# Kernel optimization log

Hardware: AMD Instinct MI355X
Metric: run time of the kernel (lower is better)

The kernel has to match this reference:

```python
import jax, jax.numpy as jnp
import numpy as np

HEADS = 8
DIM_HEAD = 64
DIM = 512
INNER = HEADS * DIM_HEAD  # 512
SCALE = DIM_HEAD ** -0.5


def setup_inputs() -> dict:
    key = jax.random.key(0)
    k1, k2, k3, k4 = jax.random.split(key, 4)
    B, N = 2, 4096
    x = jax.random.normal(k1, (B, N, DIM), dtype=jnp.float32)
    # nn.Linear(dim, inner*3, bias=False): weight [3*inner, dim]; y = x @ W.T
    w_qkv = jax.random.normal(k2, (3 * INNER, DIM), dtype=jnp.float32) * (DIM ** -0.5)
    w_out = jax.random.normal(k3, (DIM, INNER), dtype=jnp.float32) * (INNER ** -0.5)
    b_out = jax.random.normal(k4, (DIM,), dtype=jnp.float32) * 0.01
    return {"x": x, "w_qkv": w_qkv, "w_out": w_out, "b_out": b_out, "H": 64, "W": 64}


def reference(x, w_qkv, w_out, b_out, H, W):
    B, N, _ = x.shape
    qkv = jnp.einsum('bnd,ed->bne', x, w_qkv)  # [B, N, 3*inner]
    q, k, v = jnp.split(qkv, 3, axis=-1)
    def to_heads(t):
        return t.reshape(B, N, HEADS, DIM_HEAD).transpose(0, 2, 1, 3)  # b h n d
    q, k, v = to_heads(q), to_heads(k), to_heads(v)
    dots = jnp.einsum('bhid,bhjd->bhij', q, k) * SCALE
    attn = jax.nn.softmax(dots, axis=-1)  # dropout p=0.0 -> identity
    out = jnp.einsum('bhij,bhjd->bhid', attn, v)
    out = out.transpose(0, 2, 1, 3).reshape(B, N, INNER)
    return jnp.einsum('bne,de->bnd', out, w_out) + b_out
```

## Files before the change

kernel.cpp:

```cpp
#include <hip/hip_runtime.h>
#include <hip/hip_bf16.h>

typedef __hip_bfloat16 bf16;
typedef __attribute__((ext_vector_type(8))) short short8;
typedef __attribute__((ext_vector_type(4))) short shortx4;
typedef __attribute__((ext_vector_type(4))) float floatx4;
typedef __attribute__((ext_vector_type(4))) int intx4;

#define MFMA16(a, b, c) __builtin_amdgcn_mfma_f32_16x16x32_bf16((a), (b), (c), 0, 0, 0)
#define EXP2(x) __builtin_amdgcn_exp2f(x)

__device__ __forceinline__ short f2s(float v) {
    return __builtin_bit_cast(short, __float2bfloat16(v));
}

__device__ __forceinline__ int packhi(float lo, float hi) {
    return (int)__builtin_amdgcn_perm(__builtin_bit_cast(unsigned, hi),
                                      __builtin_bit_cast(unsigned, lo),
                                      0x07060302u);
}

__device__ __forceinline__ short8 cvt8v(float4 f0, float4 f1) {
    short8 r;
    r[0] = f2s(f0.x); r[1] = f2s(f0.y); r[2] = f2s(f0.z); r[3] = f2s(f0.w);
    r[4] = f2s(f1.x); r[5] = f2s(f1.y); r[6] = f2s(f1.z); r[7] = f2s(f1.w);
    return r;
}

__global__ __launch_bounds__(256) void qkv_gemm(
    const float* __restrict__ x, const float* __restrict__ wq,
    bf16* __restrict__ q, bf16* __restrict__ k, bf16* __restrict__ vt)
{
    __shared__ short pool[20480];
    short (*As)[128][40] = (short(*)[128][40])pool;
    short (*Bs)[128][40] = (short(*)[128][40])(pool + 10240);
    short (*Vt)[136] = (short(*)[136])pool;
    const int t = threadIdx.x;
    const int bm = blockIdx.x * 128;
    const int be = blockIdx.y * 128;
    const int w = t >> 6, lane = t & 63, lq = lane >> 4, lm = lane & 15;
    const int wr = w >> 1, wc = w & 1;
    const int srow = t >> 1, scol = (t & 1) * 16;
    const float C = 0.18033688011112042f;

    const float* xp = &x[(size_t)(bm + srow) * 512 + scol];
    const float* wp = &wq[(size_t)(be + srow) * 512 + scol];

    float4 xr[4], wr4[4];
    auto issue = [&](int k0) {
        const float4* a = (const float4*)(xp + k0);
        const float4* b = (const float4*)(wp + k0);
        xr[0] = a[0]; xr[1] = a[1]; xr[2] = a[2]; xr[3] = a[3];
        wr4[0] = b[0]; wr4[1] = b[1]; wr4[2] = b[2]; wr4[3] = b[3];
    };
    auto commit = [&](int buf) {
        *(short8*)&As[buf][srow][scol]     = cvt8v(xr[0], xr[1]);
        *(short8*)&As[buf][srow][scol + 8] = cvt8v(xr[2], xr[3]);
        *(short8*)&Bs[buf][srow][scol]     = cvt8v(wr4[0], wr4[1]);
        *(short8*)&Bs[buf][srow][scol + 8] = cvt8v(wr4[2], wr4[3]);
    };

    floatx4 acc[4][4];
#pragma unroll
    for (int i = 0; i < 4; ++i)
#pragma unroll
        for (int j = 0; j < 4; ++j) acc[i][j] = {0.f, 0.f, 0.f, 0.f};

    issue(0);
    commit(0);
    __syncthreads();
    int cur = 0;
    for (int k0 = 0; k0 < 512; k0 += 32) {
        const bool more = (k0 + 32) < 512;
        if (more) issue(k0 + 32);
        short8 af[4], bf[4];
#pragma unroll
        for (int mt = 0; mt < 4; ++mt) af[mt] = *(const short8*)&As[cur][wr * 64 + mt * 16 + lm][lq * 8];
#pragma unroll
        for (int nt = 0; nt < 4; ++nt) bf[nt] = *(const short8*)&Bs[cur][wc * 64 + nt * 16 + lm][lq * 8];
#pragma unroll
        for (int mt = 0; mt < 4; ++mt)
#pragma unroll
            for (int nt = 0; nt < 4; ++nt)
                acc[mt][nt] = MFMA16(af[mt], bf[nt], acc[mt][nt]);
        if (more) {
            commit(cur ^ 1);
            __syncthreads();
        }
        cur ^= 1;
    }

    const int which = be >> 9;
    if (which < 2) {
#pragma unroll
        for (int nt = 0; nt < 4; ++nt) {
            const int gcol = be + wc * 64 + nt * 16 + lm;
            const int e2 = gcol & 511;
            const int h = e2 >> 6, d = e2 & 63;
#pragma unroll
            for (int mt = 0; mt < 4; ++mt) {
#pragma unroll
                for (int r = 0; r < 4; ++r) {
                    int grow = bm + wr * 64 + mt * 16 + lq * 4 + r;
                    int b = grow >> 12, n = grow & 4095;
                    int bh = b * 8 + h;
                    float v = acc[mt][nt][r];
                    if (which == 0)
                        q[((size_t)bh * 4096 + n) * 64 + d] = __float2bfloat16(v * C);
                    else
                        k[((size_t)bh * 4096 + n) * 64 + d] = __float2bfloat16(v);
                }
            }
        }
    } else {
        __syncthreads();
#pragma unroll
        for (int nt = 0; nt < 4; ++nt) {
            const int e_loc = wc * 64 + nt * 16 + lm;
#pragma unroll
            for (int mt = 0; mt < 4; ++mt) {
                const int col = wr * 64 + 4 * (mt & 1) + 8 * lq + 32 * (mt >> 1);
                shortx4 v4;
#pragma unroll
                for (int r = 0; r < 4; ++r) v4[r] = f2s(acc[mt][nt][r]);
                *(shortx4*)&Vt[e_loc][col] = v4;
            }
        }
        __syncthreads();
        const int b = bm >> 12, n0 = bm & 4095;
        const int h0 = (be - 1024) >> 6;
        const int row = t >> 1, cb = (t & 1) * 64;
        const int h = h0 + (row >> 6), d = row & 63;
        const size_t gb = ((size_t)(b * 8 + h) * 64 + d) * 4096 + n0 + cb;
#pragma unroll
        for (int c = 0; c < 8; ++c)
            *(intx4*)&vt[gb + c * 8] = *(const intx4*)&Vt[row][cb + c * 8];
    }
}

__global__ __launch_bounds__(256, 2) void flash_attn(
    const bf16* __restrict__ q, const bf16* __restrict__ k,
    const bf16* __restrict__ vt, bf16* __restrict__ out)
{
    __shared__ short Qs[128][72];
    __shared__ short Ks[2][64][72];
    __shared__ short Vs[2][64][72];
    const int t = threadIdx.x;
    const int i0 = blockIdx.x * 128;
    const int bh = blockIdx.y;
    const int w = t >> 6, lane = t & 63, lq = lane >> 4, lm = lane & 15;
    const floatx4 zero4 = {0.f, 0.f, 0.f, 0.f};

    const size_t nbase = (size_t)bh * 4096 * 64;
    const size_t vbase = (size_t)bh * 64 * 4096;
    const int r0 = t >> 3, c0 = (t & 7) * 8;

#pragma unroll
    for (int it = 0; it < 4; ++it) {
        int off = it * 2048 + t * 8;
        int row = off >> 6, col = off & 63;
        *(intx4*)&Qs[row][col] = *(const intx4*)&q[nbase + (size_t)(i0 + row) * 64 + col];
    }

    intx4 kreg[2], vreg[2];
    auto issue = [&](int j0n) {
        kreg[0] = *(const intx4*)&k[nbase + (size_t)(j0n + r0) * 64 + c0];
        kreg[1] = *(const intx4*)&k[nbase + (size_t)(j0n + 32 + r0) * 64 + c0];
        vreg[0] = *(const intx4*)&vt[vbase + (size_t)r0 * 4096 + j0n + c0];
        vreg[1] = *(const intx4*)&vt[vbase + (size_t)(32 + r0) * 4096 + j0n + c0];
    };
    auto commit = [&](int buf) {
        *(intx4*)&Ks[buf][r0][c0]      = kreg[0];
        *(intx4*)&Ks[buf][32 + r0][c0] = kreg[1];
        *(intx4*)&Vs[buf][r0][c0]      = vreg[0];
        *(intx4*)&Vs[buf][32 + r0][c0] = vreg[1];
    };

    issue(0);
    commit(0);
    __syncthreads();
    short8 aq0[2], aq1[2];
#pragma unroll
    for (int g = 0; g < 2; ++g) {
        aq0[g] = *(const short8*)&Qs[g * 64 + w * 16 + lm][lq * 8];
        aq1[g] = *(const short8*)&Qs[g * 64 + w * 16 + lm][32 + lq * 8];
    }

    float l_lane[2] = {0.f, 0.f};
    floatx4 o_acc[2][4];
#pragma unroll
    for (int g = 0; g < 2; ++g)
#pragma unroll
        for (int dt = 0; dt < 4; ++dt) o_acc[g][dt] = zero4;

    int cur = 0;
    for (int j0 = 0; j0 < 4096; j0 += 64) {
        const bool more = (j0 + 64) < 4096;
        if (more) issue(j0 + 64);

        floatx4 s[2][4];
#pragma unroll
        for (int jt = 0; jt < 4; ++jt) {
            short8 bk0 = *(const short8*)&Ks[cur][jt * 16 + lm][lq * 8];
            short8 bk1 = *(const short8*)&Ks[cur][jt * 16 + lm][32 + lq * 8];
#pragma unroll
            for (int g = 0; g < 2; ++g) {
                s[g][jt] = MFMA16(bk0, aq0[g], zero4);
                s[g][jt] = MFMA16(bk1, aq1[g], s[g][jt]);
            }
        }

        short8 bp0[2], bp1[2];
#pragma unroll
        for (int g = 0; g < 2; ++g) {
            intx4 pkA, pkB;
#pragma unroll
            for (int jt = 0; jt < 4; ++jt) {
                float e0 = EXP2(s[g][jt][0]);
                float e1 = EXP2(s[g][jt][1]);
                float e2 = EXP2(s[g][jt][2]);
                float e3 = EXP2(s[g][jt][3]);
                l_lane[g] += (e0 + e1) + (e2 + e3);
                if (jt < 2) {
                    pkA[jt * 2]     = packhi(e0, e1);
                    pkA[jt * 2 + 1] = packhi(e2, e3);
                } else {
                    pkB[(jt - 2) * 2]     = packhi(e0, e1);
                    pkB[(jt - 2) * 2 + 1] = packhi(e2, e3);
                }
            }
            bp0[g] = __builtin_bit_cast(short8, pkA);
            bp1[g] = __builtin_bit_cast(short8, pkB);
        }

#pragma unroll
        for (int dt = 0; dt < 4; ++dt) {
            short8 av0 = *(const short8*)&Vs[cur][dt * 16 + lm][lq * 8];
            short8 av1 = *(const short8*)&Vs[cur][dt * 16 + lm][32 + lq * 8];
#pragma unroll
            for (int g = 0; g < 2; ++g) {
                o_acc[g][dt] = MFMA16(av0, bp0[g], o_acc[g][dt]);
                o_acc[g][dt] = MFMA16(av1, bp1[g], o_acc[g][dt]);
            }
        }

        if (more) {
            commit(cur ^ 1);
            __syncthreads();
        }
        cur ^= 1;
    }

    const int b = bh >> 3, h = bh & 7;
    short* Os = (short*)Qs;
    const int obase = w * 1024;
    const int il = lane >> 2, c = (lane & 3) * 16;
#pragma unroll
    for (int g = 0; g < 2; ++g) {
        float l = l_lane[g];
        l += __shfl_xor(l, 16);
        l += __shfl_xor(l, 32);
        const float inv_l = 1.0f / l;
        __syncthreads();
#pragma unroll
        for (int dt = 0; dt < 4; ++dt)
#pragma unroll
            for (int r = 0; r < 4; ++r)
                Os[obase + lm * 64 + dt * 16 + lq * 4 + r] = f2s(o_acc[g][dt][r] * inv_l);
        __syncthreads();
        const int i = i0 + g * 64 + w * 16 + il;
        intx4 v0 = *(const intx4*)&Os[obase + il * 64 + c];
        intx4 v1 = *(const intx4*)&Os[obase + il * 64 + c + 8];
        *(intx4*)&out[((size_t)b * 4096 + i) * 512 + h * 64 + c] = v0;
        *(intx4*)&out[((size_t)b * 4096 + i) * 512 + h * 64 + c + 8] = v1;
    }
}

__global__ __launch_bounds__(256) void out_gemm(
    const bf16* __restrict__ a, const float* __restrict__ wo,
    const float* __restrict__ bias, float* __restrict__ y)
{
    __shared__ short As[2][128][40];
    __shared__ short Bs[2][64][40];
    const int t = threadIdx.x;
    const int bm = blockIdx.x * 128;
    const int be = blockIdx.y * 64;
    const int w = t >> 6, lane = t & 63, lq = lane >> 4, lm = lane & 15;
    const int wr = w >> 1, wc = w & 1;
    const int srow = t >> 1, scol = (t & 1) * 16;
    const int brow = t >> 2, bcol = (t & 3) * 8;

    const bf16* ap = &a[(size_t)(bm + srow) * 512 + scol];
    const float* wp = &wo[(size_t)(be + brow) * 512 + bcol];

    intx4 ar[2];
    float4 br[2];
    auto issue = [&](int k0) {
        ar[0] = *(const intx4*)(ap + k0);
        ar[1] = *(const intx4*)(ap + k0 + 8);
        br[0] = ((const float4*)(wp + k0))[0];
        br[1] = ((const float4*)(wp + k0))[1];
    };
    auto commit = [&](int buf) {
        *(intx4*)&As[buf][srow][scol]     = ar[0];
        *(intx4*)&As[buf][srow][scol + 8] = ar[1];
        *(short8*)&Bs[buf][brow][bcol]    = cvt8v(br[0], br[1]);
    };

    floatx4 acc[4][2];
#pragma unroll
    for (int i = 0; i < 4; ++i)
#pragma unroll
        for (int j = 0; j < 2; ++j) acc[i][j] = {0.f, 0.f, 0.f, 0.f};

    issue(0);
    commit(0);
    __syncthreads();
    int cur = 0;
    for (int k0 = 0; k0 < 512; k0 += 32) {
        const bool more = (k0 + 32) < 512;
        if (more) issue(k0 + 32);
        short8 af[4], bf[2];
#pragma unroll
        for (int mt = 0; mt < 4; ++mt) af[mt] = *(const short8*)&As[cur][wr * 64 + mt * 16 + lm][lq * 8];
#pragma unroll
        for (int nt = 0; nt < 2; ++nt) bf[nt] = *(const short8*)&Bs[cur][wc * 32 + nt * 16 + lm][lq * 8];
#pragma unroll
        for (int mt = 0; mt < 4; ++mt)
#pragma unroll
            for (int nt = 0; nt < 2; ++nt)
                acc[mt][nt] = MFMA16(af[mt], bf[nt], acc[mt][nt]);
        if (more) {
            commit(cur ^ 1);
            __syncthreads();
        }
        cur ^= 1;
    }

#pragma unroll
    for (int nt = 0; nt < 2; ++nt) {
        const int gcol = be + wc * 32 + nt * 16 + lm;
        const float bv = bias[gcol];
#pragma unroll
        for (int mt = 0; mt < 4; ++mt) {
#pragma unroll
            for (int r = 0; r < 4; ++r) {
                int grow = bm + wr * 64 + mt * 16 + lq * 4 + r;
                y[(size_t)grow * 512 + gcol] = acc[mt][nt][r] + bv;
            }
        }
    }
}

extern "C" void kernel_launch(void* const* d_in, const int* in_sizes, int n_in,
                              void* d_out, int out_size, void* d_ws, size_t ws_size,
                              hipStream_t stream) {
    const float* x     = (const float*)d_in[0];
    const float* w_qkv = (const float*)d_in[1];
    const float* w_out = (const float*)d_in[2];
    const float* b_out = (const float*)d_in[3];

    const size_t HEAD_ELEMS = (size_t)16 * 4096 * 64;
    bf16* qw  = (bf16*)d_ws;
    bf16* kw  = qw + HEAD_ELEMS;
    bf16* vtw = kw + HEAD_ELEMS;
    bf16* aw  = vtw + HEAD_ELEMS;
    float* y  = (float*)d_out;

    qkv_gemm<<<dim3(64, 12), 256, 0, stream>>>(x, w_qkv, qw, kw, vtw);
    flash_attn<<<dim3(32, 16), 256, 0, stream>>>(qw, kw, vtw, aw);
    out_gemm<<<dim3(64, 8), 256, 0, stream>>>(aw, w_out, b_out, y);
}
```

Baseline: 204.6 us.

## Stage Q/K epilogue through LDS and deepen register prefetch to two tiles

The QKV GEMM epilogue for Q and K now writes the accumulator tile into shared memory and then stores whole 128-byte rows with 16-byte vector stores, replacing scattered 2-byte global writes. The attention and output-GEMM main loops keep two register stages of prefetched K/V (or A/W) data, so global loads are issued two iterations ahead instead of one. The aim is to raise store coalescing and hide more global-load latency, at the cost of extra registers (possible occupancy loss) and one extra barrier in the epilogue.

```diff
diff --git a/kernel.cpp b/kernel.cpp
--- a/kernel.cpp
+++ b/kernel.cpp
@@ -34,6 +34,7 @@
     __shared__ short pool[20480];
     short (*As)[128][40] = (short(*)[128][40])pool;
     short (*Bs)[128][40] = (short(*)[128][40])(pool + 10240);
+    short (*Qt)[144] = (short(*)[144])pool;
     short (*Vt)[136] = (short(*)[136])pool;
     const int t = threadIdx.x;
     const int bm = blockIdx.x * 128;
@@ -91,29 +92,29 @@
     }
 
     const int which = be >> 9;
+    __syncthreads();
     if (which < 2) {
+        const float scale = (which == 0) ? C : 1.0f;
 #pragma unroll
         for (int nt = 0; nt < 4; ++nt) {
-            const int gcol = be + wc * 64 + nt * 16 + lm;
-            const int e2 = gcol & 511;
-            const int h = e2 >> 6, d = e2 & 63;
-#pragma unroll
-            for (int mt = 0; mt < 4; ++mt) {
-#pragma unroll
-                for (int r = 0; r < 4; ++r) {
-                    int grow = bm + wr * 64 + mt * 16 + lq * 4 + r;
-                    int b = grow >> 12, n = grow & 4095;
-                    int bh = b * 8 + h;
-                    float v = acc[mt][nt][r];
-                    if (which == 0)
-                        q[((size_t)bh * 4096 + n) * 64 + d] = __float2bfloat16(v * C);
-                    else
-                        k[((size_t)bh * 4096 + n) * 64 + d] = __float2bfloat16(v);
-                }
-            }
-        }
+            const int e_loc = wc * 64 + nt * 16 + lm;
+#pragma unroll
+            for (int mt = 0; mt < 4; ++mt)
+#pragma unroll
+                for (int r = 0; r < 4; ++r)
+                    Qt[wr * 64 + mt * 16 + lq * 4 + r][e_loc] = f2s(acc[mt][nt][r] * scale);
+        }
+        __syncthreads();
+        bf16* dst = (which == 0) ? q : k;
+        const int tr = t >> 1, th = t & 1;
+        const int grow = bm + tr;
+        const int b = grow >> 12, n = grow & 4095;
+        const int h = ((be + th * 64) & 511) >> 6;
+        bf16* p = dst + ((size_t)(b * 8 + h) * 4096 + n) * 64;
+#pragma unroll
+        for (int c = 0; c < 8; ++c)
+            *(intx4*)&p[c * 8] = *(const intx4*)&Qt[tr][th * 64 + c * 8];
     } else {
-        __syncthreads();
 #pragma unroll
         for (int nt = 0; nt < 4; ++nt) {
             const int e_loc = wc * 64 + nt * 16 + lm;
@@ -162,22 +163,23 @@
         *(intx4*)&Qs[row][col] = *(const intx4*)&q[nbase + (size_t)(i0 + row) * 64 + col];
     }
 
-    intx4 kreg[2], vreg[2];
-    auto issue = [&](int j0n) {
-        kreg[0] = *(const intx4*)&k[nbase + (size_t)(j0n + r0) * 64 + c0];
-        kreg[1] = *(const intx4*)&k[nbase + (size_t)(j0n + 32 + r0) * 64 + c0];
-        vreg[0] = *(const intx4*)&vt[vbase + (size_t)r0 * 4096 + j0n + c0];
-        vreg[1] = *(const intx4*)&vt[vbase + (size_t)(32 + r0) * 4096 + j0n + c0];
-    };
-    auto commit = [&](int buf) {
-        *(intx4*)&Ks[buf][r0][c0]      = kreg[0];
-        *(intx4*)&Ks[buf][32 + r0][c0] = kreg[1];
-        *(intx4*)&Vs[buf][r0][c0]      = vreg[0];
-        *(intx4*)&Vs[buf][32 + r0][c0] = vreg[1];
-    };
-
-    issue(0);
-    commit(0);
+    intx4 kreg[2][2], vreg[2][2];
+    auto issue = [&](int j0n, int s) {
+        kreg[s][0] = *(const intx4*)&k[nbase + (size_t)(j0n + r0) * 64 + c0];
+        kreg[s][1] = *(const intx4*)&k[nbase + (size_t)(j0n + 32 + r0) * 64 + c0];
+        vreg[s][0] = *(const intx4*)&vt[vbase + (size_t)r0 * 4096 + j0n + c0];
+        vreg[s][1] = *(const intx4*)&vt[vbase + (size_t)(32 + r0) * 4096 + j0n + c0];
+    };
+    auto commit = [&](int s, int buf) {
+        *(intx4*)&Ks[buf][r0][c0]      = kreg[s][0];
+        *(intx4*)&Ks[buf][32 + r0][c0] = kreg[s][1];
+        *(intx4*)&Vs[buf][r0][c0]      = vreg[s][0];
+        *(intx4*)&Vs[buf][32 + r0][c0] = vreg[s][1];
+    };
+
+    issue(0, 0);
+    commit(0, 0);
+    issue(64, 1);
     __syncthreads();
     short8 aq0[2], aq1[2];
 #pragma unroll
@@ -193,10 +195,10 @@
 #pragma unroll
         for (int dt = 0; dt < 4; ++dt) o_acc[g][dt] = zero4;
 
-    int cur = 0;
-    for (int j0 = 0; j0 < 4096; j0 += 64) {
-        const bool more = (j0 + 64) < 4096;
-        if (more) issue(j0 + 64);
+    for (int i = 0; i < 64; ++i) {
+        const int j0 = i * 64;
+        const int cur = i & 1;
+        if (j0 + 128 < 4096) issue(j0 + 128, cur);
 
         floatx4 s[2][4];
 #pragma unroll
@@ -244,11 +246,10 @@
             }
         }
 
-        if (more) {
-            commit(cur ^ 1);
+        if (j0 + 64 < 4096) {
+            commit(cur ^ 1, cur ^ 1);
             __syncthreads();
         }
-        cur ^= 1;
     }
 
     const int b = bh >> 3, h = bh & 7;
@@ -293,18 +294,18 @@
     const bf16* ap = &a[(size_t)(bm + srow) * 512 + scol];
     const float* wp = &wo[(size_t)(be + brow) * 512 + bcol];
 
-    intx4 ar[2];
-    float4 br[2];
-    auto issue = [&](int k0) {
-        ar[0] = *(const intx4*)(ap + k0);
-        ar[1] = *(const intx4*)(ap + k0 + 8);
-        br[0] = ((const float4*)(wp + k0))[0];
-        br[1] = ((const float4*)(wp + k0))[1];
-    };
-    auto commit = [&](int buf) {
-        *(intx4*)&As[buf][srow][scol]     = ar[0];
-        *(intx4*)&As[buf][srow][scol + 8] = ar[1];
-        *(short8*)&Bs[buf][brow][bcol]    = cvt8v(br[0], br[1]);
+    intx4 ar[2][2];
+    float4 br[2][2];
+    auto issue = [&](int k0, int s) {
+        ar[s][0] = *(const intx4*)(ap + k0);
+        ar[s][1] = *(const intx4*)(ap + k0 + 8);
+        br[s][0] = ((const float4*)(wp + k0))[0];
+        br[s][1] = ((const float4*)(wp + k0))[1];
+    };
+    auto commit = [&](int s, int buf) {
+        *(intx4*)&As[buf][srow][scol]     = ar[s][0];
+        *(intx4*)&As[buf][srow][scol + 8] = ar[s][1];
+        *(short8*)&Bs[buf][brow][bcol]    = cvt8v(br[s][0], br[s][1]);
     };
 
     floatx4 acc[4][2];
@@ -313,13 +314,14 @@
 #pragma unroll
         for (int j = 0; j < 2; ++j) acc[i][j] = {0.f, 0.f, 0.f, 0.f};
 
-    issue(0);
-    commit(0);
+    issue(0, 0);
+    commit(0, 0);
+    issue(32, 1);
     __syncthreads();
-    int cur = 0;
-    for (int k0 = 0; k0 < 512; k0 += 32) {
-        const bool more = (k0 + 32) < 512;
-        if (more) issue(k0 + 32);
+    for (int i = 0; i < 16; ++i) {
+        const int k0 = i * 32;
+        const int cur = i & 1;
+        if (k0 + 64 < 512) issue(k0 + 64, cur);
         short8 af[4], bf[2];
 #pragma unroll
         for (int mt = 0; mt < 4; ++mt) af[mt] = *(const short8*)&As[cur][wr * 64 + mt * 16 + lm][lq * 8];
@@ -330,11 +332,10 @@
 #pragma unroll
             for (int nt = 0; nt < 2; ++nt)
                 acc[mt][nt] = MFMA16(af[mt], bf[nt], acc[mt][nt]);
-        if (more) {
-            commit(cur ^ 1);
+        if (k0 + 32 < 512) {
+            commit(cur ^ 1, cur ^ 1);
             __syncthreads();
         }
-        cur ^= 1;
     }
 
 #pragma unroll
```

Result: slower. 246.1 us (+20.3%).

## Pre-convert inputs to bf16 and stage Q/K epilogue through LDS for coalesced stores

Applied to the files above, without the earlier changes.

Adds a separate kernel that converts x, w_qkv and w_out to bf16 once, so the GEMM kernels load half the bytes and skip the per-tile float-to-bf16 conversion. Weight tiles were previously re-read and re-converted by many blocks. The Q/K epilogue now writes the accumulator tile into shared memory and then emits 16-byte row stores, replacing scattered 2-byte global writes. The trade-offs are an extra kernel launch and an extra round trip of x through memory.

```diff
diff --git a/kernel.cpp b/kernel.cpp
--- a/kernel.cpp
+++ b/kernel.cpp
@@ -27,13 +27,31 @@
     return r;
 }
 
+__global__ __launch_bounds__(256) void cvt_inputs(
+    const float* __restrict__ x, const float* __restrict__ wq,
+    const float* __restrict__ wo, bf16* __restrict__ xb,
+    bf16* __restrict__ wqb, bf16* __restrict__ wob)
+{
+    int idx = blockIdx.x * 256 + threadIdx.x;
+    const float* src;
+    bf16* dst;
+    int off;
+    if (idx < 524288)      { src = x;  dst = xb;  off = idx; }
+    else if (idx < 622592) { src = wq; dst = wqb; off = idx - 524288; }
+    else                   { src = wo; dst = wob; off = idx - 622592; }
+    float4 f0 = ((const float4*)src)[off * 2];
+    float4 f1 = ((const float4*)src)[off * 2 + 1];
+    *(short8*)&((short*)dst)[off * 8] = cvt8v(f0, f1);
+}
+
 __global__ __launch_bounds__(256) void qkv_gemm(
-    const float* __restrict__ x, const float* __restrict__ wq,
+    const bf16* __restrict__ xb, const bf16* __restrict__ wqb,
     bf16* __restrict__ q, bf16* __restrict__ k, bf16* __restrict__ vt)
 {
     __shared__ short pool[20480];
     short (*As)[128][40] = (short(*)[128][40])pool;
     short (*Bs)[128][40] = (short(*)[128][40])(pool + 10240);
+    short (*Qt)[144] = (short(*)[144])pool;
     short (*Vt)[136] = (short(*)[136])pool;
     const int t = threadIdx.x;
     const int bm = blockIdx.x * 128;
@@ -43,21 +61,21 @@
     const int srow = t >> 1, scol = (t & 1) * 16;
     const float C = 0.18033688011112042f;
 
-    const float* xp = &x[(size_t)(bm + srow) * 512 + scol];
-    const float* wp = &wq[(size_t)(be + srow) * 512 + scol];
-
-    float4 xr[4], wr4[4];
+    const bf16* xp = &xb[(size_t)(bm + srow) * 512 + scol];
+    const bf16* wp = &wqb[(size_t)(be + srow) * 512 + scol];
+
+    intx4 xr[2], wr4[2];
     auto issue = [&](int k0) {
-        const float4* a = (const float4*)(xp + k0);
-        const float4* b = (const float4*)(wp + k0);
-        xr[0] = a[0]; xr[1] = a[1]; xr[2] = a[2]; xr[3] = a[3];
-        wr4[0] = b[0]; wr4[1] = b[1]; wr4[2] = b[2]; wr4[3] = b[3];
+        xr[0] = *(const intx4*)(xp + k0);
+        xr[1] = *(const intx4*)(xp + k0 + 8);
+        wr4[0] = *(const intx4*)(wp + k0);
+        wr4[1] = *(const intx4*)(wp + k0 + 8);
     };
     auto commit = [&](int buf) {
-        *(short8*)&As[buf][srow][scol]     = cvt8v(xr[0], xr[1]);
-        *(short8*)&As[buf][srow][scol + 8] = cvt8v(xr[2], xr[3]);
-        *(short8*)&Bs[buf][srow][scol]     = cvt8v(wr4[0], wr4[1]);
-        *(short8*)&Bs[buf][srow][scol + 8] = cvt8v(wr4[2], wr4[3]);
+        *(intx4*)&As[buf][srow][scol]     = xr[0];
+        *(intx4*)&As[buf][srow][scol + 8] = xr[1];
+        *(intx4*)&Bs[buf][srow][scol]     = wr4[0];
+        *(intx4*)&Bs[buf][srow][scol + 8] = wr4[1];
     };
 
     floatx4 acc[4][4];
@@ -91,29 +109,29 @@
     }
 
     const int which = be >> 9;
+    __syncthreads();
     if (which < 2) {
+        const float scale = (which == 0) ? C : 1.0f;
 #pragma unroll
         for (int nt = 0; nt < 4; ++nt) {
-            const int gcol = be + wc * 64 + nt * 16 + lm;
-            const int e2 = gcol & 511;
-            const int h = e2 >> 6, d = e2 & 63;
-#pragma unroll
-            for (int mt = 0; mt < 4; ++mt) {
-#pragma unroll
-                for (int r = 0; r < 4; ++r) {
-                    int grow = bm + wr * 64 + mt * 16 + lq * 4 + r;
-                    int b = grow >> 12, n = grow & 4095;
-                    int bh = b * 8 + h;
-                    float v = acc[mt][nt][r];
-                    if (which == 0)
-                        q[((size_t)bh * 4096 + n) * 64 + d] = __float2bfloat16(v * C);
-                    else
-                        k[((size_t)bh * 4096 + n) * 64 + d] = __float2bfloat16(v);
-                }
-            }
-        }
+            const int e_loc = wc * 64 + nt * 16 + lm;
+#pragma unroll
+            for (int mt = 0; mt < 4; ++mt)
+#pragma unroll
+                for (int r = 0; r < 4; ++r)
+                    Qt[wr * 64 + mt * 16 + lq * 4 + r][e_loc] = f2s(acc[mt][nt][r] * scale);
+        }
+        __syncthreads();
+        bf16* dst = (which == 0) ? q : k;
+        const int tr = t >> 1, th = t & 1;
+        const int grow = bm + tr;
+        const int b = grow >> 12, n = grow & 4095;
+        const int h = ((be + th * 64) & 511) >> 6;
+        bf16* p = dst + ((size_t)(b * 8 + h) * 4096 + n) * 64;
+#pragma unroll
+        for (int c = 0; c < 8; ++c)
+            *(intx4*)&p[c * 8] = *(const intx4*)&Qt[tr][th * 64 + c * 8];
     } else {
-        __syncthreads();
 #pragma unroll
         for (int nt = 0; nt < 4; ++nt) {
             const int e_loc = wc * 64 + nt * 16 + lm;
@@ -277,7 +295,7 @@
 }
 
 __global__ __launch_bounds__(256) void out_gemm(
-    const bf16* __restrict__ a, const float* __restrict__ wo,
+    const bf16* __restrict__ a, const bf16* __restrict__ wob,
     const float* __restrict__ bias, float* __restrict__ y)
 {
     __shared__ short As[2][128][40];
@@ -291,20 +309,18 @@
     const int brow = t >> 2, bcol = (t & 3) * 8;
 
     const bf16* ap = &a[(size_t)(bm + srow) * 512 + scol];
-    const float* wp = &wo[(size_t)(be + brow) * 512 + bcol];
-
-    intx4 ar[2];
-    float4 br[2];
+    const bf16* wp = &wob[(size_t)(be + brow) * 512 + bcol];
+
+    intx4 ar[2], br;
     auto issue = [&](int k0) {
         ar[0] = *(const intx4*)(ap + k0);
         ar[1] = *(const intx4*)(ap + k0 + 8);
-        br[0] = ((const float4*)(wp + k0))[0];
-        br[1] = ((const float4*)(wp + k0))[1];
+        br    = *(const intx4*)(wp + k0);
     };
     auto commit = [&](int buf) {
         *(intx4*)&As[buf][srow][scol]     = ar[0];
         *(intx4*)&As[buf][srow][scol + 8] = ar[1];
-        *(short8*)&Bs[buf][brow][bcol]    = cvt8v(br[0], br[1]);
+        *(intx4*)&Bs[buf][brow][bcol]     = br;
     };
 
     floatx4 acc[4][2];
@@ -365,9 +381,13 @@
     bf16* kw  = qw + HEAD_ELEMS;
     bf16* vtw = kw + HEAD_ELEMS;
     bf16* aw  = vtw + HEAD_ELEMS;
+    bf16* xb  = aw + HEAD_ELEMS;
+    bf16* wqb = xb + (size_t)8192 * 512;
+    bf16* wob = wqb + (size_t)1536 * 512;
     float* y  = (float*)d_out;
 
-    qkv_gemm<<<dim3(64, 12), 256, 0, stream>>>(x, w_qkv, qw, kw, vtw);
+    cvt_inputs<<<2560, 256, 0, stream>>>(x, w_qkv, w_out, xb, wqb, wob);
+    qkv_gemm<<<dim3(64, 12), 256, 0, stream>>>(xb, wqb, qw, kw, vtw);
     flash_attn<<<dim3(32, 16), 256, 0, stream>>>(qw, kw, vtw, aw);
-    out_gemm<<<dim3(64, 8), 256, 0, stream>>>(aw, w_out, b_out, y);
-}
+    out_gemm<<<dim3(64, 8), 256, 0, stream>>>(aw, wob, b_out, y);
+}
```

Result: faster. 192.3 us (-6.0%).
